# Kernel optimization log

Hardware: AMD Instinct MI355X
Metric: run time of the kernel (lower is better)

## Reference

```python
import jax, jax.numpy as jnp
import numpy as np

K = 3            # TAGConv default number of hops
NUM_GRAPHS = 128 # graphs in the batch (for global_add_pool)


def _gcn_norm(src, dst, n):
    # PyG gcn_norm (symmetric, no self-loops): w_e = d[src]^-1/2 * d[dst]^-1/2
    deg = jnp.zeros((n,), jnp.float32).at[dst].add(1.0)
    dinv = jnp.where(deg > 0, jax.lax.rsqrt(deg), 0.0)
    return dinv[src] * dinv[dst]


def _tagconv(x, src, dst, wn, W, b):
    # out = sum_{k=0..K} (norm_adj^k x) @ W[k] + b
    n = x.shape[0]
    h = x
    out = h @ W[0]
    for k in range(1, K + 1):
        h = jax.ops.segment_sum(h[src] * wn[:, None], dst, num_segments=n)
        out = out + h @ W[k]
    return out + b


def setup_inputs() -> dict:
    key = jax.random.key(0)
    ks = jax.random.split(key, 8)
    N, E, D, H = 50000, 800000, 64, 64
    x = jax.random.normal(ks[0], (N, D), jnp.float32)
    edge_index = jax.random.randint(ks[1], (2, E), 0, N, dtype=jnp.int32)
    batch_ids = jnp.sort(jax.random.randint(ks[2], (N,), 0, NUM_GRAPHS, dtype=jnp.int32))
    def glorot(k, sh):
        return jax.random.normal(k, sh, jnp.float32) / np.float32(np.sqrt(sh[-2]))
    W0 = glorot(ks[3], (K + 1, D, H)); b0 = jnp.zeros((H,), jnp.float32)
    W1 = glorot(ks[4], (K + 1, H, H)); b1 = jnp.zeros((H,), jnp.float32)
    alpha0 = jnp.full((1,), 0.25, jnp.float32)  # PReLU default init
    alpha1 = jnp.full((1,), 0.25, jnp.float32)
    Wout = glorot(ks[5], (H, 1)); bout = jnp.zeros((1,), jnp.float32)
    return dict(x=x, edge_index=edge_index, batch_ids=batch_ids,
                W0=W0, b0=b0, W1=W1, b1=b1,
                alpha0=alpha0, alpha1=alpha1, Wout=Wout, bout=bout)


def reference(x, edge_index, batch_ids, W0, b0, W1, b1, alpha0, alpha1, Wout, bout):
    src, dst = edge_index[0], edge_index[1]
    wn = _gcn_norm(src, dst, x.shape[0])
    # layer 0: TAGConv -> (dropout=identity in eval) -> PReLU
    h = _tagconv(x, src, dst, wn, W0, b0)
    h = jnp.where(h >= 0, h, alpha0 * h)
    # layer 1
    h = _tagconv(h, src, dst, wn, W1, b1)
    h = jnp.where(h >= 0, h, alpha1 * h)
    # global_add_pool over graphs, then linear critic head
    g = jax.ops.segment_sum(h, batch_ids, num_segments=NUM_GRAPHS)  # [G, H]
    return g @ Wout + bout  # [G, 1]
```

## Files before the change

### kernel.cpp

```cpp
#include <hip/hip_runtime.h>
#include <hip/hip_bf16.h>
#include <hip/hip_fp16.h>

#define D 64
#define GRAPHS 128

using bf16x8 = __attribute__((ext_vector_type(8))) short;
using f32x4  = __attribute__((ext_vector_type(4))) float;


__device__ __forceinline__ float bf2f(unsigned short u) {
    return __uint_as_float(((unsigned)u) << 16);
}
__device__ __forceinline__ unsigned short f2bf(float f) {
    unsigned u = __float_as_uint(f);
    unsigned r = (u + 0x7FFFu + ((u >> 16) & 1u)) >> 16;
    return (unsigned short)r;
}



__global__ void prep_kernel(const int* __restrict__ dst, int* __restrict__ gcount,
                            int E, int B1,
                            const float* __restrict__ W0, const float* __restrict__ W1,
                            unsigned short* __restrict__ WF0, unsigned short* __restrict__ WF1,
                            const float* __restrict__ x, unsigned short* __restrict__ H, int NH) {
    int b = blockIdx.x;
    if (b < B1) {
        __shared__ int hist[256];
        int t = threadIdx.x;
        hist[t] = 0;
        __syncthreads();
        int e0 = b * 2048 + t;
#pragma unroll
        for (int r = 0; r < 8; ++r) {
            int e = e0 + r * 256;
            if (e < E) atomicAdd(&hist[dst[e] >> 8], 1);
        }
        __syncthreads();
        if (hist[t]) atomicAdd(&gcount[t * 32], hist[t]);
    } else if (b < B1 + 128) {
        int idx = (b - B1) * 256 + threadIdx.x;
        int i = idx & 16383;
        int j = i & 7, lane = (i >> 3) & 63, ct = (i >> 9) & 3, kt = i >> 11;
        int n = ct * 16 + (lane & 15);
        int k = kt * 32 + (lane >> 4) * 8 + j;
        if (idx < 16384) WF0[i] = f2bf(W0[k * 64 + n]);
        else             WF1[i] = f2bf(W1[k * 64 + n]);
    } else {
        int i = (b - B1 - 128) * 256 + threadIdx.x;
        if (i < NH) {
            int n = i >> 3, f = (i & 7) * 8;
            float4 x0 = *(const float4*)(x + (size_t)n * 64 + f);
            float4 x1 = *(const float4*)(x + (size_t)n * 64 + f + 4);
            bf16x8 pk;
            pk[0] = f2bf(x0.x); pk[1] = f2bf(x0.y); pk[2] = f2bf(x0.z); pk[3] = f2bf(x0.w);
            pk[4] = f2bf(x1.x); pk[5] = f2bf(x1.y); pk[6] = f2bf(x1.z); pk[7] = f2bf(x1.w);
            *(bf16x8*)(H + (size_t)n * 256 + f) = pk;
        }
    }
}


__global__ void scan256_kernel(const int* __restrict__ gcount, int* __restrict__ gbase,
                               int* __restrict__ gcursor, int E) {
    __shared__ int s[256];
    int t = threadIdx.x;
    int c = gcount[t * 32];
    s[t] = c;
    __syncthreads();
    for (int st = 1; st < 256; st <<= 1) {
        int add = (t >= st) ? s[t - st] : 0;
        __syncthreads();
        s[t] += add;
        __syncthreads();
    }
    int excl = s[t] - c;
    gbase[t] = excl;
    gcursor[t * 32] = excl;
    if (t == 255) gbase[256] = E;
}


__global__ void bucket_kernel(const int* __restrict__ dst, const int* __restrict__ src,
                              int* __restrict__ gcursor, unsigned int* __restrict__ tmp32, int E) {
    __shared__ int hist[256];
    __shared__ int basec[256];
    int t = threadIdx.x, b = blockIdx.x;
    hist[t] = 0;
    __syncthreads();
    unsigned pk[8];
    int bk[8];
    int e0 = b * 2048 + t;
#pragma unroll
    for (int r = 0; r < 8; ++r) {
        int e = e0 + r * 256;
        if (e < E) {
            int d = dst[e];
            pk[r] = ((unsigned)d << 16) | (unsigned)src[e];
            bk[r] = d >> 8;
            atomicAdd(&hist[bk[r]], 1);
        } else bk[r] = -1;
    }
    __syncthreads();
    if (hist[t]) basec[t] = atomicAdd(&gcursor[t * 32], hist[t]);
    __syncthreads();
#pragma unroll
    for (int r = 0; r < 8; ++r) {
        if (bk[r] >= 0) {
            int slot = atomicAdd(&basec[bk[r]], 1);
            tmp32[slot] = pk[r];
        }
    }
}


__global__ __launch_bounds__(512)
void radix2_kernel(const int* __restrict__ gbase, const unsigned int* __restrict__ tmp32,
                   unsigned int* __restrict__ ep, float* __restrict__ dinv,
                   int* __restrict__ pdeg, int* __restrict__ rowstart, int N) {
    __shared__ int s[256];
    __shared__ int hist[256];
    __shared__ int cur[256];
    int h = blockIdx.x, t = threadIdx.x;
    int start = gbase[h];
    int cnt   = gbase[h + 1] - start;

    if (t < 256) hist[t] = 0;
    __syncthreads();
    for (int j = t; j < cnt; j += 512)
        atomicAdd(&hist[(tmp32[start + j] >> 16) & 0xFF], 1);
    __syncthreads();

    int myc = (t < 256) ? hist[t] : 0;
    if (t < 256) s[t] = myc;
    __syncthreads();
    for (int st = 1; st < 256; st <<= 1) {
        int add = (t < 256 && t >= st) ? s[t - st] : 0;
        __syncthreads();
        if (t < 256) s[t] += add;
        __syncthreads();
    }
    if (t < 256) {
        int excl = s[t] - myc;
        int node = h * 256 + t;
        if (node < N) {
            pdeg[node] = myc;
            rowstart[node] = start + excl;
            dinv[node] = myc > 0 ? rsqrtf((float)myc) : 0.0f;
        }
        cur[t] = excl;
    }
    __syncthreads();

    for (int j = t; j < cnt; j += 512) {
        unsigned v = tmp32[start + j];
        int lo = (v >> 16) & 0xFF;
        int r = atomicAdd(&cur[lo], 1);
        ep[start + r] = v & 0xFFFFu;
    }
}


__global__ void wfix_kernel(unsigned int* __restrict__ ep, const float* __restrict__ dinv, int E) {
    int e0 = (blockIdx.x * 256 + threadIdx.x) * 4;
    if (e0 + 4 <= E) {
        uint4 v = *(const uint4*)(ep + e0);
        unsigned w0 = __half_as_ushort(__float2half(dinv[v.x]));
        unsigned w1 = __half_as_ushort(__float2half(dinv[v.y]));
        unsigned w2 = __half_as_ushort(__float2half(dinv[v.z]));
        unsigned w3 = __half_as_ushort(__float2half(dinv[v.w]));
        v.x |= w0 << 16; v.y |= w1 << 16; v.z |= w2 << 16; v.w |= w3 << 16;
        *(uint4*)(ep + e0) = v;
    } else {
        for (int e = e0; e < E; ++e) {
            unsigned v = ep[e];
            v |= (unsigned)__half_as_ushort(__float2half(dinv[v])) << 16;
            ep[e] = v;
        }
    }
}


#define GROWS 8

__global__ __launch_bounds__(512, 8)
void gather_kernel(const unsigned short* __restrict__ in,
                   unsigned short* __restrict__ out,
                   const int* __restrict__ rowstart, const int* __restrict__ pdeg,
                   const float* __restrict__ dinv, const unsigned int* __restrict__ ep, int N) {
    int wid = blockIdx.x * GROWS + (threadIdx.x >> 6);
    if (wid >= N) return;
    int lane = threadIdx.x & 63;
    int g  = lane >> 3;
    int fl = (lane & 7) * 8;

    int start = __builtin_amdgcn_readfirstlane(rowstart[wid]);
    int cnt   = __builtin_amdgcn_readfirstlane(pdeg[wid]);
    float dd  = dinv[wid];

    float a0=0.f,a1=0.f,a2=0.f,a3=0.f,a4=0.f,a5=0.f,a6=0.f,a7=0.f;
    float c0=0.f,c1=0.f,c2=0.f,c3=0.f,c4=0.f,c5=0.f,c6=0.f,c7=0.f;
    unsigned eA = 0, eB = 0;
    if (cnt > 0) {
        eA = (g < cnt) ? ep[start + g] : 0u;
        eB = (8 + g < cnt) ? ep[start + 8 + g] : 0u;
    }
    for (int i = 0; i < cnt; i += 16) {
        unsigned cA = eA, cB = eB;
        if (i + 16 < cnt) {
            eA = (i + 16 + g < cnt) ? ep[start + i + 16 + g] : 0u;
            eB = (i + 24 + g < cnt) ? ep[start + i + 24 + g] : 0u;
        }
        bf16x8 rA = *(const bf16x8*)(in + (size_t)(cA & 0xFFFFu) * 256 + fl);
        bf16x8 rB = *(const bf16x8*)(in + (size_t)(cB & 0xFFFFu) * 256 + fl);
        float wA = __half2float(__ushort_as_half((unsigned short)(cA >> 16)));
        float wB = __half2float(__ushort_as_half((unsigned short)(cB >> 16)));
        a0 = fmaf(wA, bf2f((unsigned short)rA[0]), a0);
        a1 = fmaf(wA, bf2f((unsigned short)rA[1]), a1);
        a2 = fmaf(wA, bf2f((unsigned short)rA[2]), a2);
        a3 = fmaf(wA, bf2f((unsigned short)rA[3]), a3);
        a4 = fmaf(wA, bf2f((unsigned short)rA[4]), a4);
        a5 = fmaf(wA, bf2f((unsigned short)rA[5]), a5);
        a6 = fmaf(wA, bf2f((unsigned short)rA[6]), a6);
        a7 = fmaf(wA, bf2f((unsigned short)rA[7]), a7);
        c0 = fmaf(wB, bf2f((unsigned short)rB[0]), c0);
        c1 = fmaf(wB, bf2f((unsigned short)rB[1]), c1);
        c2 = fmaf(wB, bf2f((unsigned short)rB[2]), c2);
        c3 = fmaf(wB, bf2f((unsigned short)rB[3]), c3);
        c4 = fmaf(wB, bf2f((unsigned short)rB[4]), c4);
        c5 = fmaf(wB, bf2f((unsigned short)rB[5]), c5);
        c6 = fmaf(wB, bf2f((unsigned short)rB[6]), c6);
        c7 = fmaf(wB, bf2f((unsigned short)rB[7]), c7);
    }
    a0 += c0; a1 += c1; a2 += c2; a3 += c3;
    a4 += c4; a5 += c5; a6 += c6; a7 += c7;
    a0 += __shfl_xor(a0, 8, 64); a0 += __shfl_xor(a0, 16, 64); a0 += __shfl_xor(a0, 32, 64);
    a1 += __shfl_xor(a1, 8, 64); a1 += __shfl_xor(a1, 16, 64); a1 += __shfl_xor(a1, 32, 64);
    a2 += __shfl_xor(a2, 8, 64); a2 += __shfl_xor(a2, 16, 64); a2 += __shfl_xor(a2, 32, 64);
    a3 += __shfl_xor(a3, 8, 64); a3 += __shfl_xor(a3, 16, 64); a3 += __shfl_xor(a3, 32, 64);
    a4 += __shfl_xor(a4, 8, 64); a4 += __shfl_xor(a4, 16, 64); a4 += __shfl_xor(a4, 32, 64);
    a5 += __shfl_xor(a5, 8, 64); a5 += __shfl_xor(a5, 16, 64); a5 += __shfl_xor(a5, 32, 64);
    a6 += __shfl_xor(a6, 8, 64); a6 += __shfl_xor(a6, 16, 64); a6 += __shfl_xor(a6, 32, 64);
    a7 += __shfl_xor(a7, 8, 64); a7 += __shfl_xor(a7, 16, 64); a7 += __shfl_xor(a7, 32, 64);
    if (g == 0) {
        bf16x8 pk;
        pk[0] = f2bf(a0 * dd); pk[1] = f2bf(a1 * dd);
        pk[2] = f2bf(a2 * dd); pk[3] = f2bf(a3 * dd);
        pk[4] = f2bf(a4 * dd); pk[5] = f2bf(a5 * dd);
        pk[6] = f2bf(a6 * dd); pk[7] = f2bf(a7 * dd);
        *(bf16x8*)(out + (size_t)wid * 256 + fl) = pk;
    }
}


#define LROW 72

template<int MODE>
__global__ __launch_bounds__(256, 4)
void tag_gemm_kernel(const unsigned short* __restrict__ H,
                     const unsigned short* __restrict__ Wfrag,
                     const float* __restrict__ bias, const float* __restrict__ alpha,
                     const float* __restrict__ Wout, const int* __restrict__ batch,
                     const float* __restrict__ bout,
                     unsigned short* __restrict__ H2, float* __restrict__ outp, int N) {
    __shared__ float bins[GRAPHS];
    __shared__ unsigned short lbuf[64 * LROW];
    if (MODE == 3) {
        if (threadIdx.x < GRAPHS) bins[threadIdx.x] = 0.0f;
        __syncthreads();
    }
    if (MODE == 2) {
        if (blockIdx.x == 0 && threadIdx.x < GRAPHS) outp[threadIdx.x] = bout[0];
    }

    int w = threadIdx.x >> 6, lane = threadIdx.x & 63;
    int m = lane & 15, quad = lane >> 4;
    int rowbase = blockIdx.x * 64 + w * 16;
    int arow = rowbase + m;
    size_t aoff = (size_t)min(arow, N - 1) * 256 + quad * 8;

    f32x4 acc0 = {0.f, 0.f, 0.f, 0.f}, acc1 = acc0, acc2 = acc0, acc3 = acc0;
#pragma unroll
    for (int kt = 0; kt < 8; ++kt) {
        bf16x8 A = *(const bf16x8*)(H + aoff + kt * 32);
        const unsigned short* wf = Wfrag + ((size_t)(kt * 4) * 64 + lane) * 8;
        bf16x8 B0 = *(const bf16x8*)(wf + 0 * 64 * 8);
        bf16x8 B1 = *(const bf16x8*)(wf + 1 * 64 * 8);
        bf16x8 B2 = *(const bf16x8*)(wf + 2 * 64 * 8);
        bf16x8 B3 = *(const bf16x8*)(wf + 3 * 64 * 8);
        acc0 = __builtin_amdgcn_mfma_f32_16x16x32_bf16(A, B0, acc0, 0, 0, 0);
        acc1 = __builtin_amdgcn_mfma_f32_16x16x32_bf16(A, B1, acc1, 0, 0, 0);
        acc2 = __builtin_amdgcn_mfma_f32_16x16x32_bf16(A, B2, acc2, 0, 0, 0);
        acc3 = __builtin_amdgcn_mfma_f32_16x16x32_bf16(A, B3, acc3, 0, 0, 0);
    }

    float al = alpha[0];
    f32x4 accs[4] = {acc0, acc1, acc2, acc3};
    if (MODE == 2) {
#pragma unroll
        for (int ct = 0; ct < 4; ++ct) {
            int col = ct * 16 + m;
            float b = bias[col];
#pragma unroll
            for (int r = 0; r < 4; ++r) {
                int lrow = w * 16 + quad * 4 + r;
                float v = accs[ct][r] + b;
                v = v >= 0.f ? v : al * v;
                lbuf[lrow * LROW + col] = f2bf(v);
            }
        }
        __syncthreads();
#pragma unroll
        for (int k = 0; k < 2; ++k) {
            int c = threadIdx.x * 2 + k;
            int lrow = c >> 3, part = c & 7;
            int grow = blockIdx.x * 64 + lrow;
            if (grow < N) {
                bf16x8 pk = *(const bf16x8*)(lbuf + lrow * LROW + part * 8);
                *(bf16x8*)(H2 + (size_t)grow * 256 + part * 8) = pk;
            }
        }
    } else {
        float rv0 = 0.f, rv1 = 0.f, rv2 = 0.f, rv3 = 0.f;
#pragma unroll
        for (int ct = 0; ct < 4; ++ct) {
            int col = ct * 16 + m;
            float b = bias[col], wo = Wout[col];
            float v;
            v = accs[ct][0] + b; v = v >= 0.f ? v : al * v; rv0 = fmaf(v, wo, rv0);
            v = accs[ct][1] + b; v = v >= 0.f ? v : al * v; rv1 = fmaf(v, wo, rv1);
            v = accs[ct][2] + b; v = v >= 0.f ? v : al * v; rv2 = fmaf(v, wo, rv2);
            v = accs[ct][3] + b; v = v >= 0.f ? v : al * v; rv3 = fmaf(v, wo, rv3);
        }
        float rv[4] = {rv0, rv1, rv2, rv3};
#pragma unroll
        for (int r = 0; r < 4; ++r) {
            float v = rv[r];
            v += __shfl_xor(v, 8, 16);
            v += __shfl_xor(v, 4, 16);
            v += __shfl_xor(v, 2, 16);
            v += __shfl_xor(v, 1, 16);
            int row = rowbase + quad * 4 + r;
            if (m == 0 && row < N) atomicAdd(&bins[batch[row]], v);
        }
        __syncthreads();
        if (threadIdx.x < GRAPHS) {
            float bv = bins[threadIdx.x];
            if (bv != 0.0f) atomicAdd(&outp[threadIdx.x], bv);
        }
    }
}

extern "C" void kernel_launch(void* const* d_in, const int* in_sizes, int n_in,
                              void* d_out, int out_size, void* d_ws, size_t ws_size,
                              hipStream_t stream) {
    const float* x     = (const float*)d_in[0];
    const int*   ei    = (const int*)d_in[1];
    const int*   batch = (const int*)d_in[2];
    const float* W0    = (const float*)d_in[3];
    const float* b0    = (const float*)d_in[4];
    const float* W1    = (const float*)d_in[5];
    const float* b1    = (const float*)d_in[6];
    const float* a0    = (const float*)d_in[7];
    const float* a1    = (const float*)d_in[8];
    const float* Wout  = (const float*)d_in[9];
    const float* bout  = (const float*)d_in[10];

    const int N = in_sizes[0] / D;
    const int E = in_sizes[1] / 2;
    const int* src = ei;
    const int* dst = ei + E;

    size_t off = 0;
    auto alloc = [&](size_t bytes) -> void* {
        void* p = (char*)d_ws + off;
        off = (off + bytes + 255) & ~(size_t)255;
        return p;
    };
    int*   gcount   = (int*)alloc(256 * 32 * 4);
    int*   gcursor  = (int*)alloc(256 * 32 * 4);
    int*   gbase    = (int*)alloc(257 * 4);
    int*   pdeg     = (int*)alloc((size_t)N * 4);
    int*   rowstart = (int*)alloc((size_t)N * 4);
    float* dinv     = (float*)alloc((size_t)N * 4);
    unsigned int* tmp32 = (unsigned int*)alloc((size_t)E * 4);
    unsigned int* epack = (unsigned int*)alloc((size_t)E * 4);
    unsigned short* HA = (unsigned short*)alloc((size_t)N * 256 * 2);
    unsigned short* HB = (unsigned short*)alloc((size_t)N * 256 * 2);
    unsigned short* WF0 = (unsigned short*)alloc(16384 * 2);
    unsigned short* WF1 = (unsigned short*)alloc(16384 * 2);

    const int B1  = (E + 2047) / 2048;
    const int NXH = (N * 8 + 255) / 256;
    const int NH256 = (N + 255) / 256;
    const int EB4 = (E + 1023) / 1024;
    const int NG = (N + GROWS - 1) / GROWS;
    const int NM = (N + 63) / 64;

    hipMemsetAsync(gcount, 0, 256 * 32 * 4, stream);
    prep_kernel<<<B1 + 128 + NXH, 256, 0, stream>>>(dst, gcount, E, B1,
                                                    W0, W1, WF0, WF1, x, HA, N * 8);
    scan256_kernel<<<1, 256, 0, stream>>>(gcount, gbase, gcursor, E);
    bucket_kernel<<<B1, 256, 0, stream>>>(dst, src, gcursor, tmp32, E);
    radix2_kernel<<<NH256, 512, 0, stream>>>(gbase, tmp32, epack, dinv, pdeg, rowstart, N);
    wfix_kernel<<<EB4, 256, 0, stream>>>(epack, dinv, E);

    gather_kernel<<<NG, 512, 0, stream>>>(HA + 0 * 64, HA + 1 * 64, rowstart, pdeg, dinv, epack, N);
    gather_kernel<<<NG, 512, 0, stream>>>(HA + 1 * 64, HA + 2 * 64, rowstart, pdeg, dinv, epack, N);
    gather_kernel<<<NG, 512, 0, stream>>>(HA + 2 * 64, HA + 3 * 64, rowstart, pdeg, dinv, epack, N);
    tag_gemm_kernel<2><<<NM, 256, 0, stream>>>(HA, WF0, b0, a0, nullptr, nullptr, bout,
                                               HB, (float*)d_out, N);

    gather_kernel<<<NG, 512, 0, stream>>>(HB + 0 * 64, HB + 1 * 64, rowstart, pdeg, dinv, epack, N);
    gather_kernel<<<NG, 512, 0, stream>>>(HB + 1 * 64, HB + 2 * 64, rowstart, pdeg, dinv, epack, N);
    gather_kernel<<<NG, 512, 0, stream>>>(HB + 2 * 64, HB + 3 * 64, rowstart, pdeg, dinv, epack, N);
    tag_gemm_kernel<3><<<NM, 256, 0, stream>>>(HB, WF1, b1, a1, Wout, batch, bout,
                                               nullptr, (float*)d_out, N);
}
```

Measured before the change: 258.5 us.

## Pre-scale gathered features by source dinv and drop per-edge weight packing

Instead of packing a per-edge fp16 weight dinv[src] into the edge list (the wfix kernel), each hop now reads from a compact 64-wide buffer G = dinv*h that producers write alongside H. The gather loop then uses only the source index, which removes one kernel launch and the per-edge weight decode. The gathered rows also become denser (128-byte rows instead of 512-byte strided slices), which should improve cache locality for the random reads. The cost is extra writes of the G buffers, and an additional bf16 rounding step applied to the scaled features.

```diff
diff --git a/kernel.cpp b/kernel.cpp
--- a/kernel.cpp
+++ b/kernel.cpp
@@ -38,7 +38,7 @@
             if (e < E) atomicAdd(&hist[dst[e] >> 8], 1);
         }
         __syncthreads();
-        if (hist[t]) atomicAdd(&gcount[t * 32], hist[t]);
+        if (hist[threadIdx.x]) atomicAdd(&gcount[threadIdx.x * 32], hist[threadIdx.x]);
     } else if (b < B1 + 128) {
         int idx = (b - B1) * 256 + threadIdx.x;
         int i = idx & 16383;
@@ -118,7 +118,8 @@
 __global__ __launch_bounds__(512)
 void radix2_kernel(const int* __restrict__ gbase, const unsigned int* __restrict__ tmp32,
                    unsigned int* __restrict__ ep, float* __restrict__ dinv,
-                   int* __restrict__ pdeg, int* __restrict__ rowstart, int N) {
+                   int* __restrict__ pdeg, int* __restrict__ rowstart,
+                   const unsigned short* __restrict__ h0, unsigned short* __restrict__ g0, int N) {
     __shared__ int s[256];
     __shared__ int hist[256];
     __shared__ int cur[256];
@@ -159,24 +160,17 @@
         int r = atomicAdd(&cur[lo], 1);
         ep[start + r] = v & 0xFFFFu;
     }
-}
-
-
-__global__ void wfix_kernel(unsigned int* __restrict__ ep, const float* __restrict__ dinv, int E) {
-    int e0 = (blockIdx.x * 256 + threadIdx.x) * 4;
-    if (e0 + 4 <= E) {
-        uint4 v = *(const uint4*)(ep + e0);
-        unsigned w0 = __half_as_ushort(__float2half(dinv[v.x]));
-        unsigned w1 = __half_as_ushort(__float2half(dinv[v.y]));
-        unsigned w2 = __half_as_ushort(__float2half(dinv[v.z]));
-        unsigned w3 = __half_as_ushort(__float2half(dinv[v.w]));
-        v.x |= w0 << 16; v.y |= w1 << 16; v.z |= w2 << 16; v.w |= w3 << 16;
-        *(uint4*)(ep + e0) = v;
-    } else {
-        for (int e = e0; e < E; ++e) {
-            unsigned v = ep[e];
-            v |= (unsigned)__half_as_ushort(__float2half(dinv[v])) << 16;
-            ep[e] = v;
+    __syncthreads();
+
+    for (int j = t; j < 2048; j += 512) {
+        int node = h * 256 + (j >> 3);
+        if (node < N) {
+            float dv = dinv[node];
+            bf16x8 v = *(const bf16x8*)(h0 + (size_t)node * 256 + (j & 7) * 8);
+            bf16x8 gk;
+#pragma unroll
+            for (int q = 0; q < 8; ++q) gk[q] = f2bf(bf2f((unsigned short)v[q]) * dv);
+            *(bf16x8*)(g0 + (size_t)node * 64 + (j & 7) * 8) = gk;
         }
     }
 }
@@ -185,8 +179,9 @@
 #define GROWS 8
 
 __global__ __launch_bounds__(512, 8)
-void gather_kernel(const unsigned short* __restrict__ in,
-                   unsigned short* __restrict__ out,
+void gather_kernel(const unsigned short* __restrict__ gin,
+                   unsigned short* __restrict__ hout,
+                   unsigned short* __restrict__ gout,
                    const int* __restrict__ rowstart, const int* __restrict__ pdeg,
                    const float* __restrict__ dinv, const unsigned int* __restrict__ ep, int N) {
     int wid = blockIdx.x * GROWS + (threadIdx.x >> 6);
@@ -208,14 +203,14 @@
     }
     for (int i = 0; i < cnt; i += 16) {
         unsigned cA = eA, cB = eB;
+        float wA = (i + g < cnt) ? 1.0f : 0.0f;
+        float wB = (i + 8 + g < cnt) ? 1.0f : 0.0f;
         if (i + 16 < cnt) {
             eA = (i + 16 + g < cnt) ? ep[start + i + 16 + g] : 0u;
             eB = (i + 24 + g < cnt) ? ep[start + i + 24 + g] : 0u;
         }
-        bf16x8 rA = *(const bf16x8*)(in + (size_t)(cA & 0xFFFFu) * 256 + fl);
-        bf16x8 rB = *(const bf16x8*)(in + (size_t)(cB & 0xFFFFu) * 256 + fl);
-        float wA = __half2float(__ushort_as_half((unsigned short)(cA >> 16)));
-        float wB = __half2float(__ushort_as_half((unsigned short)(cB >> 16)));
+        bf16x8 rA = *(const bf16x8*)(gin + (size_t)cA * 64 + fl);
+        bf16x8 rB = *(const bf16x8*)(gin + (size_t)cB * 64 + fl);
         a0 = fmaf(wA, bf2f((unsigned short)rA[0]), a0);
         a1 = fmaf(wA, bf2f((unsigned short)rA[1]), a1);
         a2 = fmaf(wA, bf2f((unsigned short)rA[2]), a2);
@@ -244,12 +239,18 @@
     a6 += __shfl_xor(a6, 8, 64); a6 += __shfl_xor(a6, 16, 64); a6 += __shfl_xor(a6, 32, 64);
     a7 += __shfl_xor(a7, 8, 64); a7 += __shfl_xor(a7, 16, 64); a7 += __shfl_xor(a7, 32, 64);
     if (g == 0) {
+        float h0 = a0 * dd, h1 = a1 * dd, h2 = a2 * dd, h3 = a3 * dd;
+        float h4 = a4 * dd, h5 = a5 * dd, h6 = a6 * dd, h7 = a7 * dd;
         bf16x8 pk;
-        pk[0] = f2bf(a0 * dd); pk[1] = f2bf(a1 * dd);
-        pk[2] = f2bf(a2 * dd); pk[3] = f2bf(a3 * dd);
-        pk[4] = f2bf(a4 * dd); pk[5] = f2bf(a5 * dd);
-        pk[6] = f2bf(a6 * dd); pk[7] = f2bf(a7 * dd);
-        *(bf16x8*)(out + (size_t)wid * 256 + fl) = pk;
+        pk[0] = f2bf(h0); pk[1] = f2bf(h1); pk[2] = f2bf(h2); pk[3] = f2bf(h3);
+        pk[4] = f2bf(h4); pk[5] = f2bf(h5); pk[6] = f2bf(h6); pk[7] = f2bf(h7);
+        *(bf16x8*)(hout + (size_t)wid * 256 + fl) = pk;
+        if (gout) {
+            bf16x8 gk;
+            gk[0] = f2bf(h0 * dd); gk[1] = f2bf(h1 * dd); gk[2] = f2bf(h2 * dd); gk[3] = f2bf(h3 * dd);
+            gk[4] = f2bf(h4 * dd); gk[5] = f2bf(h5 * dd); gk[6] = f2bf(h6 * dd); gk[7] = f2bf(h7 * dd);
+            *(bf16x8*)(gout + (size_t)wid * 64 + fl) = gk;
+        }
     }
 }
 
@@ -262,8 +263,9 @@
                      const unsigned short* __restrict__ Wfrag,
                      const float* __restrict__ bias, const float* __restrict__ alpha,
                      const float* __restrict__ Wout, const int* __restrict__ batch,
-                     const float* __restrict__ bout,
-                     unsigned short* __restrict__ H2, float* __restrict__ outp, int N) {
+                     const float* __restrict__ bout, const float* __restrict__ dinvp,
+                     unsigned short* __restrict__ H2, unsigned short* __restrict__ Gout,
+                     float* __restrict__ outp, int N) {
     __shared__ float bins[GRAPHS];
     __shared__ unsigned short lbuf[64 * LROW];
     if (MODE == 3) {
@@ -319,6 +321,11 @@
             if (grow < N) {
                 bf16x8 pk = *(const bf16x8*)(lbuf + lrow * LROW + part * 8);
                 *(bf16x8*)(H2 + (size_t)grow * 256 + part * 8) = pk;
+                float dv = dinvp[grow];
+                bf16x8 gk;
+#pragma unroll
+                for (int q = 0; q < 8; ++q) gk[q] = f2bf(bf2f((unsigned short)pk[q]) * dv);
+                *(bf16x8*)(Gout + (size_t)grow * 64 + part * 8) = gk;
             }
         }
     } else {
@@ -388,13 +395,14 @@
     unsigned int* epack = (unsigned int*)alloc((size_t)E * 4);
     unsigned short* HA = (unsigned short*)alloc((size_t)N * 256 * 2);
     unsigned short* HB = (unsigned short*)alloc((size_t)N * 256 * 2);
+    unsigned short* G0 = (unsigned short*)alloc((size_t)N * 64 * 2);
+    unsigned short* G1 = (unsigned short*)alloc((size_t)N * 64 * 2);
     unsigned short* WF0 = (unsigned short*)alloc(16384 * 2);
     unsigned short* WF1 = (unsigned short*)alloc(16384 * 2);
 
     const int B1  = (E + 2047) / 2048;
     const int NXH = (N * 8 + 255) / 256;
     const int NH256 = (N + 255) / 256;
-    const int EB4 = (E + 1023) / 1024;
     const int NG = (N + GROWS - 1) / GROWS;
     const int NM = (N + 63) / 64;
 
@@ -403,18 +411,18 @@
                                                     W0, W1, WF0, WF1, x, HA, N * 8);
     scan256_kernel<<<1, 256, 0, stream>>>(gcount, gbase, gcursor, E);
     bucket_kernel<<<B1, 256, 0, stream>>>(dst, src, gcursor, tmp32, E);
-    radix2_kernel<<<NH256, 512, 0, stream>>>(gbase, tmp32, epack, dinv, pdeg, rowstart, N);
-    wfix_kernel<<<EB4, 256, 0, stream>>>(epack, dinv, E);
-
-    gather_kernel<<<NG, 512, 0, stream>>>(HA + 0 * 64, HA + 1 * 64, rowstart, pdeg, dinv, epack, N);
-    gather_kernel<<<NG, 512, 0, stream>>>(HA + 1 * 64, HA + 2 * 64, rowstart, pdeg, dinv, epack, N);
-    gather_kernel<<<NG, 512, 0, stream>>>(HA + 2 * 64, HA + 3 * 64, rowstart, pdeg, dinv, epack, N);
-    tag_gemm_kernel<2><<<NM, 256, 0, stream>>>(HA, WF0, b0, a0, nullptr, nullptr, bout,
-                                               HB, (float*)d_out, N);
-
-    gather_kernel<<<NG, 512, 0, stream>>>(HB + 0 * 64, HB + 1 * 64, rowstart, pdeg, dinv, epack, N);
-    gather_kernel<<<NG, 512, 0, stream>>>(HB + 1 * 64, HB + 2 * 64, rowstart, pdeg, dinv, epack, N);
-    gather_kernel<<<NG, 512, 0, stream>>>(HB + 2 * 64, HB + 3 * 64, rowstart, pdeg, dinv, epack, N);
-    tag_gemm_kernel<3><<<NM, 256, 0, stream>>>(HB, WF1, b1, a1, Wout, batch, bout,
-                                               nullptr, (float*)d_out, N);
-}
+    radix2_kernel<<<NH256, 512, 0, stream>>>(gbase, tmp32, epack, dinv, pdeg, rowstart,
+                                             HA, G0, N);
+
+    gather_kernel<<<NG, 512, 0, stream>>>(G0, HA + 1 * 64, G1, rowstart, pdeg, dinv, epack, N);
+    gather_kernel<<<NG, 512, 0, stream>>>(G1, HA + 2 * 64, G0, rowstart, pdeg, dinv, epack, N);
+    gather_kernel<<<NG, 512, 0, stream>>>(G0, HA + 3 * 64, nullptr, rowstart, pdeg, dinv, epack, N);
+    tag_gemm_kernel<2><<<NM, 256, 0, stream>>>(HA, WF0, b0, a0, nullptr, nullptr, bout, dinv,
+                                               HB, G0, (float*)d_out, N);
+
+    gather_kernel<<<NG, 512, 0, stream>>>(G0, HB + 1 * 64, G1, rowstart, pdeg, dinv, epack, N);
+    gather_kernel<<<NG, 512, 0, stream>>>(G1, HB + 2 * 64, G0, rowstart, pdeg, dinv, epack, N);
+    gather_kernel<<<NG, 512, 0, stream>>>(G0, HB + 3 * 64, nullptr, rowstart, pdeg, dinv, epack, N);
+    tag_gemm_kernel<3><<<NM, 256, 0, stream>>>(HB, WF1, b1, a1, Wout, batch, bout, dinv,
+                                               nullptr, nullptr, (float*)d_out, N);
+}
```

After: 263.0 us. No clear change (+1.7%).
